# Optimization experiments

Hardware: AMD Instinct MI355X
Metric: run time of the kernel (lower is better)

## Reference

```python
import jax, jax.numpy as jnp
import numpy as np

N_NODES = 100000
N_EDGES = 1600000
N_GRAPHS = 64
VOCAB = 50000
D = 128
EPS = 1e-5


def setup_inputs() -> dict:
    key = jax.random.key(0)
    ks = jax.random.split(key, 24)
    tokens = jax.random.randint(ks[0], (N_NODES,), 0, VOCAB)
    src = jax.random.randint(ks[1], (N_EDGES,), 0, N_NODES)
    dst = jax.random.randint(ks[2], (N_EDGES,), 0, N_NODES)
    graph_ids = jnp.sort(jax.random.randint(ks[3], (N_NODES,), 0, N_GRAPHS))
    s = 1.0 / np.sqrt(D)
    inp = {
        'tokens': tokens, 'src': src, 'dst': dst, 'graph_ids': graph_ids,
        'embed': jax.random.normal(ks[4], (VOCAB, D), jnp.float32),
        'W1': jax.random.normal(ks[5], (D, D), jnp.float32) * s,
        'b1': jnp.zeros((D,), jnp.float32),
        'g1': jnp.ones((D,), jnp.float32), 'be1': jnp.zeros((D,), jnp.float32),
        'W2': jax.random.normal(ks[6], (D, D), jnp.float32) * s,
        'b2': jnp.zeros((D,), jnp.float32),
        'g2': jnp.ones((D,), jnp.float32), 'be2': jnp.zeros((D,), jnp.float32),
        'W3': jax.random.normal(ks[7], (D, D), jnp.float32) * s,
        'b3': jnp.zeros((D,), jnp.float32),
        'g3': jnp.ones((D,), jnp.float32), 'be3': jnp.zeros((D,), jnp.float32),
        'fcW1': jax.random.normal(ks[8], (D, D // 2), jnp.float32) * s,
        'fcb1': jnp.zeros((D // 2,), jnp.float32),
        'fcW2': jax.random.normal(ks[9], (D // 2, 2), jnp.float32) * (1.0 / np.sqrt(D // 2)),
        'fcb2': jnp.zeros((2,), jnp.float32),
    }
    return inp


def _graph_conv(h, src, dst, norm_src, norm_dst, W, b):
    # DGL GraphConv, norm='both': D_out^{-1/2} -> sum-aggregate -> D_in^{-1/2} -> linear
    msg = (h * norm_src[:, None])[src]                      # [E, D]
    agg = jax.ops.segment_sum(msg, dst, num_segments=N_NODES)
    return (agg * norm_dst[:, None]) @ W + b


def _bn_relu(h, gamma, beta):
    mu = jnp.mean(h, axis=0)
    var = jnp.mean((h - mu) ** 2, axis=0)                   # biased var (torch BN)
    return jax.nn.relu((h - mu) * jax.lax.rsqrt(var + EPS) * gamma + beta)


def reference(tokens, src, dst, graph_ids, embed,
              W1, b1, g1, be1, W2, b2, g2, be2, W3, b3, g3, be3,
              fcW1, fcb1, fcW2, fcb2):
    ones_e = jnp.ones((N_EDGES,), jnp.float32)
    deg_out = jnp.maximum(jax.ops.segment_sum(ones_e, src, num_segments=N_NODES), 1.0)
    deg_in = jnp.maximum(jax.ops.segment_sum(ones_e, dst, num_segments=N_NODES), 1.0)
    norm_src = jax.lax.rsqrt(deg_out)
    norm_dst = jax.lax.rsqrt(deg_in)

    h = embed[tokens]                                        # [N, D]
    h = _bn_relu(_graph_conv(h, src, dst, norm_src, norm_dst, W1, b1), g1, be1)
    h = _bn_relu(_graph_conv(h, src, dst, norm_src, norm_dst, W2, b2), g2, be2)
    h = _bn_relu(_graph_conv(h, src, dst, norm_src, norm_dst, W3, b3), g3, be3)

    # dgl.mean_nodes per graph
    sums = jax.ops.segment_sum(h, graph_ids, num_segments=N_GRAPHS)  # [G, D]
    cnts = jnp.maximum(jax.ops.segment_sum(jnp.ones((N_NODES,), jnp.float32), graph_ids, num_segments=N_GRAPHS), 1.0)
    hg = sums / cnts[:, None]

    hg = jax.nn.relu(hg @ fcW1 + fcb1)                       # dropout = identity (eval)
    return hg @ fcW2 + fcb2                                  # [G, 2]
```

## Files before the change

### kernel.cpp

```cpp
#include <hip/hip_runtime.h>

#define N_NODES 100000
#define N_EDGES 1600000
#define N_GRAPHS 64
#define DIM 128
#define BN_EPS 1e-5f
#define EPAD 2000000

#define NB_DEG 6250
#define NB_EMB 6250
#define NB_SENT 977
#define NB_WPREP 192
#define NB_HIST 391
#define NBUCK 782
#define NG (NBUCK * NB_HIST)
#define NB_SCANG 1195
#define BUCK_RESERVE 388

#define AT_STRIDE 136

typedef unsigned short ushort_t;
typedef unsigned char uchar_t;
typedef unsigned int uint_t;
typedef __attribute__((ext_vector_type(8))) short bf16x8;
typedef __attribute__((ext_vector_type(4))) float f32x4;

__device__ __forceinline__ float bfl(uint_t u) {
    union { uint_t i; float f; } v; v.i = u << 16; return v.f;
}
__device__ __forceinline__ float bfh(uint_t u) {
    union { uint_t i; float f; } v; v.i = u & 0xffff0000u; return v.f;
}
__device__ __forceinline__ ushort_t f2bf(float f) {
    union { float f; uint_t i; } v; v.f = f;
    uint_t x = v.i;
    return (ushort_t)((x + 0x7fffu + ((x >> 16) & 1u)) >> 16);
}
__device__ __forceinline__ uint_t pack2(float lo, float hi) {
    return ((uint_t)f2bf(hi) << 16) | (uint_t)f2bf(lo);
}

__global__ void k_zero(int* __restrict__ p, int n) {
    int i = blockIdx.x * blockDim.x + threadIdx.x;
    if (i < n) p[i] = 0;
}

__global__ void k_front(const int* __restrict__ src, const int* __restrict__ dst,
                        int* __restrict__ dego,
                        const int* __restrict__ tokens, const float* __restrict__ embed,
                        ushort_t* __restrict__ bufH, ushort_t* __restrict__ bufY,
                        ushort_t* __restrict__ bufZ, int* __restrict__ esrc,
                        const float* __restrict__ w1, const float* __restrict__ w2,
                        const float* __restrict__ w3, ushort_t* __restrict__ wbt,
                        int* __restrict__ G) {
    __shared__ int hh[NBUCK];
    int b = blockIdx.x;
    int t = threadIdx.x;
    if (b < NB_DEG) {
        int e = b * 256 + t;
        if (e < N_EDGES) atomicAdd(&dego[src[e]], 1);
        return;
    }
    b -= NB_DEG;
    if (b < NB_EMB) {
        int gid = b * 256 + t;
        int node = gid >> 4, sub = gid & 15;
        const float* ep = embed + (size_t)tokens[node] * DIM + sub * 8;
        float4 a = *(const float4*)ep;
        float4 c = *(const float4*)(ep + 4);
        uint4 o;
        o.x = pack2(a.x, a.y); o.y = pack2(a.z, a.w);
        o.z = pack2(c.x, c.y); o.w = pack2(c.z, c.w);
        *(uint4*)(bufH + (size_t)node * DIM + sub * 8) = o;
        return;
    }
    b -= NB_EMB;
    if (b < NB_SENT) {
        int i0 = (b * 256 + t) * 8;
        int4 sv = make_int4(N_NODES, N_NODES, N_NODES, N_NODES);
        if (i0 + 8 <= EPAD) {
            *(int4*)(esrc + i0) = sv;
            *(int4*)(esrc + i0 + 4) = sv;
        } else {
            for (int i = i0; i < EPAD; ++i) esrc[i] = N_NODES;
        }
        if (b == 0 && t < 64) {
            ((uint_t*)(bufH + (size_t)N_NODES * DIM))[t] = 0u;
            ((uint_t*)(bufY + (size_t)N_NODES * DIM))[t] = 0u;
            ((uint_t*)(bufZ + (size_t)N_NODES * DIM))[t] = 0u;
        }
        return;
    }
    b -= NB_SENT;
    if (b < NB_WPREP) {
        int i = b * 256 + t;
        int l = i >> 14;
        int idx = i & (DIM * DIM - 1);
        int n = idx >> 7, k = idx & (DIM - 1);
        const float* wsrc = (l == 0) ? w1 : (l == 1) ? w2 : w3;
        wbt[i] = f2bf(wsrc[k * DIM + n]);
        return;
    }
    b -= NB_WPREP;
    {
        for (int k = t; k < NBUCK; k += 256) hh[k] = 0;
        __syncthreads();
        int e0 = b * 4096;
        int e1 = min(e0 + 4096, N_EDGES);
        for (int i = e0 + t; i < e1; i += 256) atomicAdd(&hh[dst[i] >> 7], 1);
        __syncthreads();
        for (int k = t; k < NBUCK; k += 256) G[k * NB_HIST + b] = hh[k];
    }
}

__global__ void k_scanA(const int* __restrict__ G, int* __restrict__ Gs,
                        int* __restrict__ partials) {
    __shared__ int s[256];
    int t = threadIdx.x;
    int i = blockIdx.x * 256 + t;
    int v = (i < NG) ? G[i] : 0;
    s[t] = v;
    __syncthreads();
    for (int off = 1; off < 256; off <<= 1) {
        int add = (t >= off) ? s[t - off] : 0;
        __syncthreads();
        s[t] += add;
        __syncthreads();
    }
    if (i < NG) Gs[i + 1] = s[t];
    if (t == 255) partials[blockIdx.x] = s[t];
}

__global__ void k_scanB(const int* __restrict__ partials, int* __restrict__ Gs) {
    __shared__ int s[256];
    int t = threadIdx.x;
    int p = 0;
    for (int j = t; j < (int)blockIdx.x; j += 256) p += partials[j];
    s[t] = p;
    __syncthreads();
    for (int off = 128; off > 0; off >>= 1) {
        if (t < off) s[t] += s[t + off];
        __syncthreads();
    }
    int prefix = s[0];
    int i = blockIdx.x * 256 + t;
    if (i < NG) Gs[i + 1] += prefix;
    if (blockIdx.x == 0 && t == 0) Gs[0] = 0;
}

__global__ void k_pass2(const int* __restrict__ src, const int* __restrict__ dst,
                        const int* __restrict__ Gs, int* __restrict__ Csrc,
                        uchar_t* __restrict__ Cdl) {
    __shared__ int cur[NBUCK];
    int b = blockIdx.x;
    int t = threadIdx.x;
    for (int k = t; k < NBUCK; k += 256) cur[k] = Gs[k * NB_HIST + b];
    __syncthreads();
    int e0 = b * 4096;
    int e1 = min(e0 + 4096, N_EDGES);
    for (int i = e0 + t; i < e1; i += 256) {
        int d = dst[i];
        int slot = atomicAdd(&cur[d >> 7], 1);
        Csrc[slot] = src[i];
        Cdl[slot] = (uchar_t)(d & 127);
    }
}

__global__ void k_fine(const int* __restrict__ Csrc, const uchar_t* __restrict__ Cdl,
                       const int* __restrict__ Gs, const int* __restrict__ dego,
                       int* __restrict__ esrc, int* __restrict__ rowptr,
                       int* __restrict__ pdeg, float* __restrict__ ns,
                       float* __restrict__ nd) {
    __shared__ int hcnt[128];
    __shared__ int hstart[128];
    int k = blockIdx.x;
    int t = threadIdx.x;
    int node0 = k * 128;
    int nn = min(128, N_NODES - node0);
    int S = Gs[k * NB_HIST];
    int E = Gs[(k + 1) * NB_HIST];
    if (t < 128) hcnt[t] = 0;
    __syncthreads();
    for (int i = S + t; i < E; i += 256) atomicAdd(&hcnt[Cdl[i]], 1);
    __syncthreads();
    if (t == 0) {
        int acc = 0;
        for (int n = 0; n < nn; ++n) {
            hstart[n] = acc;
            acc += (hcnt[n] + 3) & ~3;
        }
    }
    __syncthreads();
    int base = (k * BUCK_RESERVE + S + 3) & ~3;
    if (t < nn) {
        int node = node0 + t;
        rowptr[node] = base + hstart[t];
        pdeg[node] = (hcnt[t] + 3) & ~3;
        nd[node] = rsqrtf(fmaxf((float)hcnt[t], 1.0f));
        ns[node] = rsqrtf(fmaxf((float)dego[node], 1.0f));
    }
    if (k == 0 && t == 0) ns[N_NODES] = 0.f;
    __syncthreads();
    for (int i = S + t; i < E; i += 256) {
        int slot = atomicAdd(&hstart[Cdl[i]], 1);
        esrc[base + slot] = Csrc[i];
    }
}

template <int DOBN>
__global__ __launch_bounds__(256) void k_agggemm(const ushort_t* __restrict__ hs,
        const int* __restrict__ rowptr, const int* __restrict__ pdeg,
        const int* __restrict__ esrc,
        const float* __restrict__ ns, const float* __restrict__ nd,
        const float* __restrict__ pbnsum, const float* __restrict__ pbnsq,
        const float* __restrict__ pg, const float* __restrict__ pbe,
        const ushort_t* __restrict__ wbt, const float* __restrict__ bias,
        ushort_t* __restrict__ y,
        float* __restrict__ bnsum, float* __restrict__ bnsq) {
    __shared__ ushort_t at[64 * AT_STRIDE];
    __shared__ float sa[DIM], sc[DIM];
    __shared__ float csum[DIM], csq[DIM];
    int tid = threadIdx.x;
    if (tid < DIM) {
        csum[tid] = 0.f; csq[tid] = 0.f;
        if (DOBN) {
            float mu = pbnsum[tid] * (1.0f / N_NODES);
            float var = pbnsq[tid] * (1.0f / N_NODES) - mu * mu;
            float rstd = rsqrtf(var + BN_EPS);
            float a = pg[tid] * rstd;
            sa[tid] = a;
            sc[tid] = pbe[tid] - mu * a;
        }
    }
    __syncthreads();

    int wave = tid >> 6;
    int lane = tid & 63;
    int bnode = blockIdx.x * 64 + wave * 16;
    int off = lane * 2;
    float a0 = 0.f, a1 = 0.f, c0 = 0.f, c1 = 0.f;
    if (DOBN) { a0 = sa[off]; a1 = sa[off + 1]; c0 = sc[off]; c1 = sc[off + 1]; }

    int rpv = 0, pdv = 0;
    if (lane < 16) {
        int nnode = bnode + lane;
        if (nnode < N_NODES) { rpv = rowptr[nnode]; pdv = pdeg[nnode]; }
    }

    for (int i = 0; i < 16; ++i) {
        int node = bnode + i;
        uint_t ov = 0u;
        int beg = __shfl(rpv, i);
        int end = beg + __shfl(pdv, i);
        if (node < N_NODES) {
            float ax0 = 0.f, ay0 = 0.f, ax1 = 0.f, ay1 = 0.f;
            float ax2 = 0.f, ay2 = 0.f, ax3 = 0.f, ay3 = 0.f;

#define AGG_ONE(U, N, AX, AY)                                                  \
    {                                                                          \
        float vl = bfl(U), vh = bfh(U);                                        \
        if (DOBN) {                                                            \
            vl = fmaxf(fmaf(vl, a0, c0), 0.f);                                 \
            vh = fmaxf(fmaf(vh, a1, c1), 0.f);                                 \
        }                                                                      \
        AX = fmaf(vl, N, AX); AY = fmaf(vh, N, AY);                            \
    }
            int e = beg;
            for (; e + 8 <= end; e += 8) {
                int4 i0 = *(const int4*)(esrc + e);
                int4 i1 = *(const int4*)(esrc + e + 4);
                uint_t u0 = *(const uint_t*)(hs + (size_t)i0.x * DIM + off);
                uint_t u1 = *(const uint_t*)(hs + (size_t)i0.y * DIM + off);
                uint_t u2 = *(const uint_t*)(hs + (size_t)i0.z * DIM + off);
                uint_t u3 = *(const uint_t*)(hs + (size_t)i0.w * DIM + off);
                uint_t u4 = *(const uint_t*)(hs + (size_t)i1.x * DIM + off);
                uint_t u5 = *(const uint_t*)(hs + (size_t)i1.y * DIM + off);
                uint_t u6 = *(const uint_t*)(hs + (size_t)i1.z * DIM + off);
                uint_t u7 = *(const uint_t*)(hs + (size_t)i1.w * DIM + off);
                float n0 = ns[i0.x], n1 = ns[i0.y], n2 = ns[i0.z], n3 = ns[i0.w];
                float n4 = ns[i1.x], n5 = ns[i1.y], n6 = ns[i1.z], n7 = ns[i1.w];
                AGG_ONE(u0, n0, ax0, ay0);
                AGG_ONE(u1, n1, ax1, ay1);
                AGG_ONE(u2, n2, ax2, ay2);
                AGG_ONE(u3, n3, ax3, ay3);
                AGG_ONE(u4, n4, ax0, ay0);
                AGG_ONE(u5, n5, ax1, ay1);
                AGG_ONE(u6, n6, ax2, ay2);
                AGG_ONE(u7, n7, ax3, ay3);
            }
            if (e < end) {
                int4 i0 = *(const int4*)(esrc + e);
                uint_t u0 = *(const uint_t*)(hs + (size_t)i0.x * DIM + off);
                uint_t u1 = *(const uint_t*)(hs + (size_t)i0.y * DIM + off);
                uint_t u2 = *(const uint_t*)(hs + (size_t)i0.z * DIM + off);
                uint_t u3 = *(const uint_t*)(hs + (size_t)i0.w * DIM + off);
                float n0 = ns[i0.x], n1 = ns[i0.y], n2 = ns[i0.z], n3 = ns[i0.w];
                AGG_ONE(u0, n0, ax0, ay0);
                AGG_ONE(u1, n1, ax1, ay1);
                AGG_ONE(u2, n2, ax2, ay2);
                AGG_ONE(u3, n3, ax3, ay3);
            }
#undef AGG_ONE
            float ax = (ax0 + ax1) + (ax2 + ax3);
            float ay = (ay0 + ay1) + (ay2 + ay3);
            float n = nd[node];
            ov = pack2(ax * n, ay * n);
        }
        *(uint_t*)&at[(wave * 16 + i) * AT_STRIDE + off] = ov;
    }
    __syncthreads();

    int m16 = lane & 15;
    int quad = lane >> 4;
    f32x4 acc[8];
#pragma unroll
    for (int nb = 0; nb < 8; ++nb) acc[nb] = (f32x4)(0.f);

    const ushort_t* ap = &at[(wave * 16 + m16) * AT_STRIDE + quad * 8];
#pragma unroll
    for (int k0b = 0; k0b < 4; ++k0b) {
        bf16x8 af = *(const bf16x8*)(ap + k0b * 32);
#pragma unroll
        for (int nb = 0; nb < 8; ++nb) {
            int ncol = nb * 16 + m16;
            bf16x8 bfg = *(const bf16x8*)(wbt + (size_t)ncol * DIM + k0b * 32 + quad * 8);
            acc[nb] = __builtin_amdgcn_mfma_f32_16x16x32_bf16(af, bfg, acc[nb], 0, 0, 0);
        }
    }

#pragma unroll
    for (int nb = 0; nb < 8; ++nb) {
        int col = nb * 16 + m16;
        float bcol = bias[col];
        float ps = 0.f, pq = 0.f;
#pragma unroll
        for (int reg = 0; reg < 4; ++reg) {
            int r = bnode + quad * 4 + reg;
            if (r < N_NODES) {
                float v = acc[nb][reg] + bcol;
                ps += v; pq += v * v;
                y[(size_t)r * DIM + col] = f2bf(v);
            }
        }
        atomicAdd(&csum[col], ps);
        atomicAdd(&csq[col], pq);
    }
    __syncthreads();
    if (tid < DIM) {
        atomicAdd(&bnsum[tid], csum[tid]);
        atomicAdd(&bnsq[tid], csq[tid]);
    }
}

#define POOL_NODES 128
__global__ void k_pool(const ushort_t* __restrict__ yin, const int* __restrict__ gids,
                       const float* __restrict__ bnsum, const float* __restrict__ bnsq,
                       const float* __restrict__ g, const float* __restrict__ be,
                       float* __restrict__ pool, int* __restrict__ cnt) {
    __shared__ int h[N_GRAPHS];
    int col = threadIdx.x;
    float mu = bnsum[col] * (1.0f / N_NODES);
    float var = bnsq[col] * (1.0f / N_NODES) - mu * mu;
    float rstd = rsqrtf(var + BN_EPS);
    float a = g[col] * rstd;
    float c = be[col] - mu * a;
    if (col < N_GRAPHS) h[col] = 0;
    __syncthreads();
    int base = blockIdx.x * POOL_NODES;
    int end = min(base + POOL_NODES, N_NODES);
    for (int n = base + col; n < end; n += 128) atomicAdd(&h[gids[n]], 1);
    __syncthreads();
    if (col < N_GRAPHS && h[col]) atomicAdd(&cnt[col], h[col]);
    float acc = 0.f;
    int cur = gids[base];
    for (int n = base; n < end; ++n) {
        int gg = gids[n];
        if (gg != cur) {
            atomicAdd(&pool[(size_t)cur * DIM + col], acc);
            acc = 0.f;
            cur = gg;
        }
        uint_t u = *(const uint_t*)(yin + (size_t)n * DIM + (col & ~1));
        float v = (col & 1) ? bfh(u) : bfl(u);
        acc += fmaxf(fmaf(v, a, c), 0.f);
    }
    atomicAdd(&pool[(size_t)cur * DIM + col], acc);
}

__global__ void k_final(const float* __restrict__ pool, const int* __restrict__ cnt,
                        const float* __restrict__ fcW1, const float* __restrict__ fcb1,
                        const float* __restrict__ fcW2, const float* __restrict__ fcb2,
                        float* __restrict__ out) {
    __shared__ float hg[DIM];
    __shared__ float z[64];
    int g = blockIdx.x;
    int t = threadIdx.x;
    float cf = fmaxf((float)cnt[g], 1.0f);
    hg[t] = pool[(size_t)g * DIM + t] / cf;
    __syncthreads();
    if (t < 64) {
        float acc = fcb1[t];
        for (int k = 0; k < DIM; ++k)
            acc += hg[k] * fcW1[k * 64 + t];
        z[t] = fmaxf(acc, 0.f);
    }
    __syncthreads();
    if (t < 2) {
        float acc = fcb2[t];
        for (int k = 0; k < 64; ++k)
            acc += z[k] * fcW2[k * 2 + t];
        out[g * 2 + t] = acc;
    }
}

extern "C" void kernel_launch(void* const* d_in, const int* in_sizes, int n_in,
                              void* d_out, int out_size, void* d_ws, size_t ws_size,
                              hipStream_t stream) {
    const int* tokens = (const int*)d_in[0];
    const int* src = (const int*)d_in[1];
    const int* dst = (const int*)d_in[2];
    const int* gids = (const int*)d_in[3];
    const float* embed = (const float*)d_in[4];
    const float* W1 = (const float*)d_in[5];
    const float* b1 = (const float*)d_in[6];
    const float* g1 = (const float*)d_in[7];
    const float* be1 = (const float*)d_in[8];
    const float* W2 = (const float*)d_in[9];
    const float* b2 = (const float*)d_in[10];
    const float* g2 = (const float*)d_in[11];
    const float* be2 = (const float*)d_in[12];
    const float* W3 = (const float*)d_in[13];
    const float* b3 = (const float*)d_in[14];
    const float* g3 = (const float*)d_in[15];
    const float* be3 = (const float*)d_in[16];
    const float* fcW1 = (const float*)d_in[17];
    const float* fcb1 = (const float*)d_in[18];
    const float* fcW2 = (const float*)d_in[19];
    const float* fcb2 = (const float*)d_in[20];
    float* out = (float*)d_out;

    char* w = (char*)d_ws;
    auto alloc = [&](size_t bytes) {
        void* p = (void*)w;
        w += (bytes + 255) & ~(size_t)255;
        return p;
    };
    ushort_t* bufH = (ushort_t*)alloc((size_t)(N_NODES + 1) * DIM * 2);
    ushort_t* bufY = (ushort_t*)alloc((size_t)(N_NODES + 1) * DIM * 2);
    ushort_t* bufZ = (ushort_t*)alloc((size_t)(N_NODES + 1) * DIM * 2);
    int* esrc = (int*)alloc((size_t)EPAD * 4);
    int* rowptr = (int*)alloc((size_t)N_NODES * 4);
    int* pdeg = (int*)alloc((size_t)N_NODES * 4);
    float* ns = (float*)alloc((size_t)(N_NODES + 1) * 4);
    float* nd = (float*)alloc((size_t)N_NODES * 4);
    ushort_t* wbt = (ushort_t*)alloc(3 * DIM * DIM * 2);
    int* G = (int*)alloc((size_t)NG * 4);
    int* Gs = (int*)alloc((size_t)(NG + 1) * 4);
    int* partials = (int*)alloc(2048 * 4);
    int* Csrc = (int*)alloc((size_t)N_EDGES * 4);
    uchar_t* Cdl = (uchar_t*)alloc((size_t)N_EDGES);
    char* zstart = w;
    int* dego = (int*)alloc((size_t)N_NODES * 4);
    float* bnsum = (float*)alloc(3 * DIM * 4);
    float* bnsq = (float*)alloc(3 * DIM * 4);
    float* pool = (float*)alloc((size_t)N_GRAPHS * DIM * 4);
    int* cnt = (int*)alloc((size_t)N_GRAPHS * 4);
    int zwords = (int)((size_t)(w - zstart) / 4);

    k_zero<<<(zwords + 255) / 256, 256, 0, stream>>>((int*)zstart, zwords);
    k_front<<<NB_DEG + NB_EMB + NB_SENT + NB_WPREP + NB_HIST, 256, 0, stream>>>(
        src, dst, dego, tokens, embed, bufH, bufY, bufZ, esrc, W1, W2, W3, wbt, G);
    k_scanA<<<NB_SCANG, 256, 0, stream>>>(G, Gs, partials);
    k_scanB<<<NB_SCANG, 256, 0, stream>>>(partials, Gs);
    k_pass2<<<NB_HIST, 256, 0, stream>>>(src, dst, Gs, Csrc, Cdl);
    k_fine<<<NBUCK, 256, 0, stream>>>(Csrc, Cdl, Gs, dego, esrc, rowptr, pdeg, ns, nd);

    int nb_fused = (N_NODES + 63) / 64;

    k_agggemm<0><<<nb_fused, 256, 0, stream>>>(
        bufH, rowptr, pdeg, esrc, ns, nd, nullptr, nullptr, nullptr, nullptr,
        wbt, b1, bufY, bnsum, bnsq);
    k_agggemm<1><<<nb_fused, 256, 0, stream>>>(
        bufY, rowptr, pdeg, esrc, ns, nd, bnsum, bnsq, g1, be1,
        wbt + (size_t)DIM * DIM, b2, bufZ, bnsum + DIM, bnsq + DIM);
    k_agggemm<1><<<nb_fused, 256, 0, stream>>>(
        bufZ, rowptr, pdeg, esrc, ns, nd, bnsum + DIM, bnsq + DIM, g2, be2,
        wbt + (size_t)2 * DIM * DIM, b3, bufY, bnsum + 2 * DIM, bnsq + 2 * DIM);

    k_pool<<<(N_NODES + POOL_NODES - 1) / POOL_NODES, DIM, 0, stream>>>(
        bufY, gids, bnsum + 2 * DIM, bnsq + 2 * DIM, g3, be3, pool, cnt);
    k_final<<<N_GRAPHS, DIM, 0, stream>>>(pool, cnt, fcW1, fcb1, fcW2, fcb2, out);
}
```

Measured before the change: 722.1 us.

## Pre-apply BN-ReLU and source norm per node before edge aggregation

```diff
diff --git a/kernel.cpp b/kernel.cpp
--- a/kernel.cpp
+++ b/kernel.cpp
@@ -48,8 +48,8 @@
 __global__ void k_front(const int* __restrict__ src, const int* __restrict__ dst,
                         int* __restrict__ dego,
                         const int* __restrict__ tokens, const float* __restrict__ embed,
-                        ushort_t* __restrict__ bufH, ushort_t* __restrict__ bufY,
-                        ushort_t* __restrict__ bufZ, int* __restrict__ esrc,
+                        ushort_t* __restrict__ bufH, ushort_t* __restrict__ bufA,
+                        int* __restrict__ esrc,
                         const float* __restrict__ w1, const float* __restrict__ w2,
                         const float* __restrict__ w3, ushort_t* __restrict__ wbt,
                         int* __restrict__ G) {
@@ -84,11 +84,8 @@
         } else {
             for (int i = i0; i < EPAD; ++i) esrc[i] = N_NODES;
         }
-        if (b == 0 && t < 64) {
-            ((uint_t*)(bufH + (size_t)N_NODES * DIM))[t] = 0u;
-            ((uint_t*)(bufY + (size_t)N_NODES * DIM))[t] = 0u;
-            ((uint_t*)(bufZ + (size_t)N_NODES * DIM))[t] = 0u;
-        }
+        if (b == 0 && t < 64)
+            ((uint_t*)(bufA + (size_t)N_NODES * DIM))[t] = 0u;
         return;
     }
     b -= NB_SENT;
@@ -208,38 +205,59 @@
 }
 
 template <int DOBN>
+__global__ void k_prescale(const ushort_t* __restrict__ yin, const float* __restrict__ ns,
+                           const float* __restrict__ bnsum, const float* __restrict__ bnsq,
+                           const float* __restrict__ g, const float* __restrict__ be,
+                           ushort_t* __restrict__ xout) {
+    __shared__ float sa[DIM], sc[DIM];
+    int t = threadIdx.x;
+    if (DOBN) {
+        if (t < DIM) {
+            float mu = bnsum[t] * (1.0f / N_NODES);
+            float var = bnsq[t] * (1.0f / N_NODES) - mu * mu;
+            float rstd = rsqrtf(var + BN_EPS);
+            float a = g[t] * rstd;
+            sa[t] = a;
+            sc[t] = be[t] - mu * a;
+        }
+        __syncthreads();
+    }
+    int gid = blockIdx.x * 256 + t;
+    int node = gid >> 4, sub = gid & 15;
+    float s = ns[node];
+    uint4 u = *(const uint4*)(yin + (size_t)node * DIM + sub * 8);
+    float v[8] = {bfl(u.x), bfh(u.x), bfl(u.y), bfh(u.y),
+                  bfl(u.z), bfh(u.z), bfl(u.w), bfh(u.w)};
+    if (DOBN) {
+        const float* a = sa + sub * 8;
+        const float* c = sc + sub * 8;
+#pragma unroll
+        for (int i = 0; i < 8; ++i) v[i] = fmaxf(fmaf(v[i], a[i], c[i]), 0.f);
+    }
+#pragma unroll
+    for (int i = 0; i < 8; ++i) v[i] *= s;
+    uint4 o;
+    o.x = pack2(v[0], v[1]); o.y = pack2(v[2], v[3]);
+    o.z = pack2(v[4], v[5]); o.w = pack2(v[6], v[7]);
+    *(uint4*)(xout + (size_t)node * DIM + sub * 8) = o;
+}
+
 __global__ __launch_bounds__(256) void k_agggemm(const ushort_t* __restrict__ hs,
         const int* __restrict__ rowptr, const int* __restrict__ pdeg,
-        const int* __restrict__ esrc,
-        const float* __restrict__ ns, const float* __restrict__ nd,
-        const float* __restrict__ pbnsum, const float* __restrict__ pbnsq,
-        const float* __restrict__ pg, const float* __restrict__ pbe,
+        const int* __restrict__ esrc, const float* __restrict__ nd,
         const ushort_t* __restrict__ wbt, const float* __restrict__ bias,
         ushort_t* __restrict__ y,
         float* __restrict__ bnsum, float* __restrict__ bnsq) {
     __shared__ ushort_t at[64 * AT_STRIDE];
-    __shared__ float sa[DIM], sc[DIM];
     __shared__ float csum[DIM], csq[DIM];
     int tid = threadIdx.x;
-    if (tid < DIM) {
-        csum[tid] = 0.f; csq[tid] = 0.f;
-        if (DOBN) {
-            float mu = pbnsum[tid] * (1.0f / N_NODES);
-            float var = pbnsq[tid] * (1.0f / N_NODES) - mu * mu;
-            float rstd = rsqrtf(var + BN_EPS);
-            float a = pg[tid] * rstd;
-            sa[tid] = a;
-            sc[tid] = pbe[tid] - mu * a;
-        }
-    }
+    if (tid < DIM) { csum[tid] = 0.f; csq[tid] = 0.f; }
     __syncthreads();
 
     int wave = tid >> 6;
     int lane = tid & 63;
     int bnode = blockIdx.x * 64 + wave * 16;
     int off = lane * 2;
-    float a0 = 0.f, a1 = 0.f, c0 = 0.f, c1 = 0.f;
-    if (DOBN) { a0 = sa[off]; a1 = sa[off + 1]; c0 = sc[off]; c1 = sc[off + 1]; }
 
     int rpv = 0, pdv = 0;
     if (lane < 16) {
@@ -255,16 +273,6 @@
         if (node < N_NODES) {
             float ax0 = 0.f, ay0 = 0.f, ax1 = 0.f, ay1 = 0.f;
             float ax2 = 0.f, ay2 = 0.f, ax3 = 0.f, ay3 = 0.f;
-
-#define AGG_ONE(U, N, AX, AY)                                                  \
-    {                                                                          \
-        float vl = bfl(U), vh = bfh(U);                                        \
-        if (DOBN) {                                                            \
-            vl = fmaxf(fmaf(vl, a0, c0), 0.f);                                 \
-            vh = fmaxf(fmaf(vh, a1, c1), 0.f);                                 \
-        }                                                                      \
-        AX = fmaf(vl, N, AX); AY = fmaf(vh, N, AY);                            \
-    }
             int e = beg;
             for (; e + 8 <= end; e += 8) {
                 int4 i0 = *(const int4*)(esrc + e);
@@ -277,16 +285,14 @@
                 uint_t u5 = *(const uint_t*)(hs + (size_t)i1.y * DIM + off);
                 uint_t u6 = *(const uint_t*)(hs + (size_t)i1.z * DIM + off);
                 uint_t u7 = *(const uint_t*)(hs + (size_t)i1.w * DIM + off);
-                float n0 = ns[i0.x], n1 = ns[i0.y], n2 = ns[i0.z], n3 = ns[i0.w];
-                float n4 = ns[i1.x], n5 = ns[i1.y], n6 = ns[i1.z], n7 = ns[i1.w];
-                AGG_ONE(u0, n0, ax0, ay0);
-                AGG_ONE(u1, n1, ax1, ay1);
-                AGG_ONE(u2, n2, ax2, ay2);
-                AGG_ONE(u3, n3, ax3, ay3);
-                AGG_ONE(u4, n4, ax0, ay0);
-                AGG_ONE(u5, n5, ax1, ay1);
-                AGG_ONE(u6, n6, ax2, ay2);
-                AGG_ONE(u7, n7, ax3, ay3);
+                ax0 += bfl(u0); ay0 += bfh(u0);
+                ax1 += bfl(u1); ay1 += bfh(u1);
+                ax2 += bfl(u2); ay2 += bfh(u2);
+                ax3 += bfl(u3); ay3 += bfh(u3);
+                ax0 += bfl(u4); ay0 += bfh(u4);
+                ax1 += bfl(u5); ay1 += bfh(u5);
+                ax2 += bfl(u6); ay2 += bfh(u6);
+                ax3 += bfl(u7); ay3 += bfh(u7);
             }
             if (e < end) {
                 int4 i0 = *(const int4*)(esrc + e);
@@ -294,13 +300,11 @@
                 uint_t u1 = *(const uint_t*)(hs + (size_t)i0.y * DIM + off);
                 uint_t u2 = *(const uint_t*)(hs + (size_t)i0.z * DIM + off);
                 uint_t u3 = *(const uint_t*)(hs + (size_t)i0.w * DIM + off);
-                float n0 = ns[i0.x], n1 = ns[i0.y], n2 = ns[i0.z], n3 = ns[i0.w];
-                AGG_ONE(u0, n0, ax0, ay0);
-                AGG_ONE(u1, n1, ax1, ay1);
-                AGG_ONE(u2, n2, ax2, ay2);
-                AGG_ONE(u3, n3, ax3, ay3);
+                ax0 += bfl(u0); ay0 += bfh(u0);
+                ax1 += bfl(u1); ay1 += bfh(u1);
+                ax2 += bfl(u2); ay2 += bfh(u2);
+                ax3 += bfl(u3); ay3 += bfh(u3);
             }
-#undef AGG_ONE
             float ax = (ax0 + ax1) + (ax2 + ax3);
             float ay = (ay0 + ay1) + (ay2 + ay3);
             float n = nd[node];
@@ -446,8 +450,8 @@
         return p;
     };
     ushort_t* bufH = (ushort_t*)alloc((size_t)(N_NODES + 1) * DIM * 2);
+    ushort_t* bufA = (ushort_t*)alloc((size_t)(N_NODES + 1) * DIM * 2);
     ushort_t* bufY = (ushort_t*)alloc((size_t)(N_NODES + 1) * DIM * 2);
-    ushort_t* bufZ = (ushort_t*)alloc((size_t)(N_NODES + 1) * DIM * 2);
     int* esrc = (int*)alloc((size_t)EPAD * 4);
     int* rowptr = (int*)alloc((size_t)N_NODES * 4);
     int* pdeg = (int*)alloc((size_t)N_NODES * 4);
@@ -469,23 +473,26 @@
 
     k_zero<<<(zwords + 255) / 256, 256, 0, stream>>>((int*)zstart, zwords);
     k_front<<<NB_DEG + NB_EMB + NB_SENT + NB_WPREP + NB_HIST, 256, 0, stream>>>(
-        src, dst, dego, tokens, embed, bufH, bufY, bufZ, esrc, W1, W2, W3, wbt, G);
+        src, dst, dego, tokens, embed, bufH, bufA, esrc, W1, W2, W3, wbt, G);
     k_scanA<<<NB_SCANG, 256, 0, stream>>>(G, Gs, partials);
     k_scanB<<<NB_SCANG, 256, 0, stream>>>(partials, Gs);
     k_pass2<<<NB_HIST, 256, 0, stream>>>(src, dst, Gs, Csrc, Cdl);
     k_fine<<<NBUCK, 256, 0, stream>>>(Csrc, Cdl, Gs, dego, esrc, rowptr, pdeg, ns, nd);
 
     int nb_fused = (N_NODES + 63) / 64;
-
-    k_agggemm<0><<<nb_fused, 256, 0, stream>>>(
-        bufH, rowptr, pdeg, esrc, ns, nd, nullptr, nullptr, nullptr, nullptr,
-        wbt, b1, bufY, bnsum, bnsq);
-    k_agggemm<1><<<nb_fused, 256, 0, stream>>>(
-        bufY, rowptr, pdeg, esrc, ns, nd, bnsum, bnsq, g1, be1,
-        wbt + (size_t)DIM * DIM, b2, bufZ, bnsum + DIM, bnsq + DIM);
-    k_agggemm<1><<<nb_fused, 256, 0, stream>>>(
-        bufZ, rowptr, pdeg, esrc, ns, nd, bnsum + DIM, bnsq + DIM, g2, be2,
-        wbt + (size_t)2 * DIM * DIM, b3, bufY, bnsum + 2 * DIM, bnsq + 2 * DIM);
+    int nb_ps = 6250;
+
+    k_prescale<0><<<nb_ps, 256, 0, stream>>>(bufH, ns, nullptr, nullptr, nullptr, nullptr, bufA);
+    k_agggemm<<<nb_fused, 256, 0, stream>>>(bufA, rowptr, pdeg, esrc, nd,
+                                            wbt, b1, bufY, bnsum, bnsq);
+    k_prescale<1><<<nb_ps, 256, 0, stream>>>(bufY, ns, bnsum, bnsq, g1, be1, bufA);
+    k_agggemm<<<nb_fused, 256, 0, stream>>>(bufA, rowptr, pdeg, esrc, nd,
+                                            wbt + (size_t)DIM * DIM, b2, bufH,
+                                            bnsum + DIM, bnsq + DIM);
+    k_prescale<1><<<nb_ps, 256, 0, stream>>>(bufH, ns, bnsum + DIM, bnsq + DIM, g2, be2, bufA);
+    k_agggemm<<<nb_fused, 256, 0, stream>>>(bufA, rowptr, pdeg, esrc, nd,
+                                            wbt + (size_t)2 * DIM * DIM, b3, bufY,
+                                            bnsum + 2 * DIM, bnsq + 2 * DIM);
 
     k_pool<<<(N_NODES + POOL_NODES - 1) / POOL_NODES, DIM, 0, stream>>>(
         bufY, gids, bnsum + 2 * DIM, bnsq + 2 * DIM, g3, be3, pool, cnt);
```

Result: slower. 739.0 us (+2.3%).
